# Performance work log

Measured on AMD Instinct MI355X. Metric: run time of the kernel, lower is better.

Reference implementation:

```python
import jax, jax.numpy as jnp
import numpy as np

H = 16          # num_heads
K = 15          # kernel_size (padding_l = K-1, causal)
EPS = 1e-5      # LayerNorm eps


def setup_inputs() -> dict:
    key = jax.random.key(0)
    ks = jax.random.split(key, 8)
    T, B, C, F = 1024, 8, 1024, 4096
    n = lambda k, shape, scale=1.0: jax.random.normal(k, shape, jnp.float32) * scale
    return {
        "x": n(ks[0], (T, B, C)),
        "w_lin": n(ks[1], (C, H * K), 0.02),      # dynamic-conv weight projection
        "b_lin": jnp.zeros((H * K,), jnp.float32),
        "ln_g": jnp.ones((C,), jnp.float32),
        "ln_b": jnp.zeros((C,), jnp.float32),
        "fc1_w": n(ks[2], (C, F), 0.02),
        "fc1_b": jnp.zeros((F,), jnp.float32),
        "fc2_w": n(ks[3], (F, C), 0.02),
        "fc2_b": jnp.zeros((C,), jnp.float32),
    }


def _dynamic_conv(x, w_lin, b_lin):
    # x: (T, B, C). Per-timestep weights -> softmax over kernel -> causal conv.
    T, B, C = x.shape
    R = C // H  # channels per head
    w = jnp.einsum('tbc,ck->tbk', x, w_lin) + b_lin          # (T, B, H*K)
    w = jax.nn.softmax(w.reshape(T, B, H, K), axis=-1)        # softmax over kernel taps
    # causal left-padding: tap k sees x[t + k - (K-1)]
    xp = jnp.pad(x, ((K - 1, 0), (0, 0), (0, 0))).reshape(T + K - 1, B, H, R)
    o = jnp.zeros((T, B, H, R), x.dtype)
    for k in range(K):  # fixed small kernel loop; avoids (T,B,C,K) unfold tensor
        o = o + w[:, :, :, k:k + 1] * xp[k:k + T]
    return o.reshape(T, B, C)


def _layer_norm(y, g, b):
    mu = jnp.mean(y, axis=-1, keepdims=True)
    var = jnp.var(y, axis=-1, keepdims=True)
    return (y - mu) * jax.lax.rsqrt(var + EPS) * g + b


def _forward(x, w_lin, b_lin, ln_g, ln_b, fc1_w, fc1_b, fc2_w, fc2_b):
    y = _dynamic_conv(x, w_lin, b_lin)
    y = _layer_norm(y, ln_g, ln_b)
    h = jax.nn.relu(jnp.einsum('tbc,cf->tbf', y, fc1_w) + fc1_b)
    out = jnp.einsum('tbf,fc->tbc', h, fc2_w) + fc2_b
    return out + y  # residual around FFN (residual taken post-LayerNorm)


def reference(x, w_lin, b_lin, ln_g, ln_b, fc1_w, fc1_b, fc2_w, fc2_b):
    return _forward(x, w_lin, b_lin, ln_g, ln_b, fc1_w, fc1_b, fc2_w, fc2_b)
```

## Files before the change

kernel.cpp:

```cpp
#include <hip/hip_runtime.h>


#define T_DIM 1024
#define B_DIM 8
#define C_DIM 1024
#define F_DIM 4096
#define H_DIM 16
#define K_TAP 15
#define TB (T_DIM * B_DIM)

typedef __attribute__((ext_vector_type(8))) short short8;
typedef __attribute__((ext_vector_type(4))) float f32x4;

__device__ __forceinline__ float bf2f(unsigned short u) {
    union { unsigned int i; float f; } v; v.i = ((unsigned int)u) << 16; return v.f;
}
__device__ __forceinline__ unsigned short f2bf(float f) {
    union { float f; unsigned int i; } v; v.f = f;
    unsigned int r = v.i + 0x7fffu + ((v.i >> 16) & 1u);
    return (unsigned short)(r >> 16);
}

__device__ __forceinline__ void async_copy16(const void* gptr, void* lptr) {
    __builtin_amdgcn_global_load_lds(
        (const __attribute__((address_space(1))) void*)gptr,
        (__attribute__((address_space(3))) void*)lptr, 16, 0, 0);
}

__global__ __launch_bounds__(256)
void prep(const float* __restrict__ x, unsigned short* __restrict__ xb,
          const float* __restrict__ fc1_w, unsigned short* __restrict__ fc1T,
          const float* __restrict__ fc2_w, unsigned short* __restrict__ fc2T,
          const float* __restrict__ w_lin, unsigned short* __restrict__ wlinT) {
    const int bid = blockIdx.x;
    const int tid = threadIdx.x;
    if (bid < 8192) {
        int i = (bid * 256 + tid) * 4;
        float4 v = *(const float4*)(x + i);
        uint2 o;
        o.x = (unsigned int)f2bf(v.x) | ((unsigned int)f2bf(v.y) << 16);
        o.y = (unsigned int)f2bf(v.z) | ((unsigned int)f2bf(v.w) << 16);
        *(uint2*)(xb + i) = o;
        return;
    }
    const float* in; unsigned short* out; int R, Cin, c0, r0;
    if (bid < 12288) {
        int idx = bid - 8192;
        in = fc1_w; out = fc1T; R = C_DIM; Cin = F_DIM;
        c0 = (idx & 127) * 32; r0 = (idx >> 7) * 32;
    } else if (bid < 16384) {
        int idx = bid - 12288;
        in = fc2_w; out = fc2T; R = F_DIM; Cin = C_DIM;
        c0 = (idx & 31) * 32; r0 = (idx >> 5) * 32;
    } else {
        int idx = bid - 16384;
        in = w_lin; out = wlinT; R = C_DIM; Cin = 240;
        c0 = (idx & 7) * 32; r0 = (idx >> 3) * 32;
    }
    __shared__ unsigned short tile[32][33];
    const int xx = tid & 31, yy = tid >> 5;
#pragma unroll
    for (int j = 0; j < 4; j++) {
        int r = r0 + yy + j * 8, c = c0 + xx;
        unsigned short v = 0;
        if (c < Cin) v = f2bf(in[(size_t)r * Cin + c]);
        tile[yy + j * 8][xx] = v;
    }
    __syncthreads();
#pragma unroll
    for (int j = 0; j < 4; j++) {
        out[(size_t)(c0 + yy + j * 8) * R + (r0 + xx)] = tile[xx][yy + j * 8];
    }
}

template <int MODE, int SWAP>
__global__ __launch_bounds__(256)
void gemm_bt(const unsigned short* __restrict__ A,
             const unsigned short* __restrict__ Bt,
             void* __restrict__ Cout_v,
             int M, int N, int K, int kz,
             const float* __restrict__ bias,
             const unsigned short* __restrict__ resid) {
    __shared__ __align__(16) unsigned short As[2][128 * 64];
    __shared__ __align__(16) unsigned short Bs[2][128 * 64];

    const int tid = threadIdx.x;
    const int m0 = (SWAP ? blockIdx.x : blockIdx.y) * 128;
    const int n0 = (SWAP ? blockIdx.y : blockIdx.x) * 128;
    const int kbase = blockIdx.z * kz;
    const int wave = tid >> 6, lane = tid & 63;
    const int quad = lane >> 4, l16 = lane & 15;
    const int wm = (wave >> 1) * 64;
    const int wn = (wave & 1) * 64;

    f32x4 acc[4][4];
#pragma unroll
    for (int i = 0; i < 4; i++)
#pragma unroll
        for (int j = 0; j < 4; j++) acc[i][j] = (f32x4){0.f, 0.f, 0.f, 0.f};

    const int rsub = lane >> 3;
    const int gch = (lane & 7) ^ rsub;
    const unsigned short* gA = A + (size_t)(m0 + wave * 32 + rsub) * K + kbase + gch * 8;
    const unsigned short* gB = Bt + (size_t)(n0 + wave * 32 + rsub) * K + kbase + gch * 8;
    unsigned short* lA[2] = {&As[0][wave * 32 * 64], &As[1][wave * 32 * 64]};
    unsigned short* lB[2] = {&Bs[0][wave * 32 * 64], &Bs[1][wave * 32 * 64]};

#pragma unroll
    for (int j = 0; j < 4; j++) {
        async_copy16(gA + (size_t)j * 8 * K, lA[0] + j * 8 * 64);
        async_copy16(gB + (size_t)j * 8 * K, lB[0] + j * 8 * 64);
    }

    const int swz = l16 & 7;
    int buf = 0;
    for (int k0 = 0; k0 < kz; k0 += 64) {
        __syncthreads();

        const int nk = k0 + 64;
        if (nk < kz) {
            const int nb = buf ^ 1;
#pragma unroll
            for (int j = 0; j < 4; j++) {
                async_copy16(gA + nk + (size_t)j * 8 * K, lA[nb] + j * 8 * 64);
                async_copy16(gB + nk + (size_t)j * 8 * K, lB[nb] + j * 8 * 64);
            }
        }

        short8 af[2][4], bfr[2][4];
#pragma unroll
        for (int kk = 0; kk < 2; kk++) {
            const int c = kk * 4 + quad;
#pragma unroll
            for (int i = 0; i < 4; i++) {
                af[kk][i]  = *(const short8*)(&As[buf][(wm + i * 16 + l16) * 64 + (c ^ swz) * 8]);
                bfr[kk][i] = *(const short8*)(&Bs[buf][(wn + i * 16 + l16) * 64 + (c ^ swz) * 8]);
            }
        }
#pragma unroll
        for (int kk = 0; kk < 2; kk++)
#pragma unroll
            for (int mi = 0; mi < 4; mi++)
#pragma unroll
                for (int nj = 0; nj < 4; nj++)
                    acc[mi][nj] = __builtin_amdgcn_mfma_f32_16x16x32_bf16(
                        af[kk][mi], bfr[kk][nj], acc[mi][nj], 0, 0, 0);
        buf ^= 1;
    }

    const int crow0 = m0 + wm + quad * 4;
    const int ccol0 = n0 + wn + l16;
    if (MODE == 3) {
        float* Cf = (float*)Cout_v + (size_t)blockIdx.z * M * N;
#pragma unroll
        for (int mi = 0; mi < 4; mi++)
#pragma unroll
            for (int i = 0; i < 4; i++) {
                int rr = crow0 + mi * 16 + i;
#pragma unroll
                for (int nj = 0; nj < 4; nj++)
                    Cf[(size_t)rr * N + ccol0 + nj * 16] = acc[mi][nj][i];
            }
    } else if (MODE == 1) {
        unsigned short* Cb = (unsigned short*)Cout_v;
        float bv[4];
#pragma unroll
        for (int nj = 0; nj < 4; nj++) bv[nj] = bias[ccol0 + nj * 16];
#pragma unroll
        for (int mi = 0; mi < 4; mi++)
#pragma unroll
            for (int i = 0; i < 4; i++) {
                int rr = crow0 + mi * 16 + i;
#pragma unroll
                for (int nj = 0; nj < 4; nj++) {
                    float v = fmaxf(acc[mi][nj][i] + bv[nj], 0.f);
                    Cb[(size_t)rr * N + ccol0 + nj * 16] = f2bf(v);
                }
            }
    } else {
        float* Cf = (float*)Cout_v;
        float bv[4];
#pragma unroll
        for (int nj = 0; nj < 4; nj++) bv[nj] = bias[ccol0 + nj * 16];
#pragma unroll
        for (int mi = 0; mi < 4; mi++)
#pragma unroll
            for (int i = 0; i < 4; i++) {
                int rr = crow0 + mi * 16 + i;
#pragma unroll
                for (int nj = 0; nj < 4; nj++) {
                    float v = acc[mi][nj][i] + bv[nj]
                            + bf2f(resid[(size_t)rr * N + ccol0 + nj * 16]);
                    Cf[(size_t)rr * N + ccol0 + nj * 16] = v;
                }
            }
    }
}

#define WS_STRIDE ((size_t)TB * 256)
__global__ __launch_bounds__(256)
void conv_ln8s(const unsigned short* __restrict__ x,
               const float* __restrict__ wscore,
               const float* __restrict__ b_lin,
               const float* __restrict__ ln_g,
               const float* __restrict__ ln_b,
               unsigned short* __restrict__ y) {
    __shared__ __align__(16) unsigned short xs[22][C_DIM];
    __shared__ float wls[8 * 240];
    const int blk = blockIdx.x;
    const int b = blk & 7;
    const int t0 = (blk >> 3) * 8;
    const int tid = threadIdx.x;

    if (tid < 128) {
        const int rj = tid >> 4, hh = tid & 15;
        const size_t row = (size_t)(t0 + rj) * B_DIM + b;
        const float* p = wscore + row * 256 + hh * 15;
        float v[K_TAP], mx = -1e30f;
#pragma unroll
        for (int k = 0; k < K_TAP; k++) {
            v[k] = p[k] + p[k + WS_STRIDE] + p[k + 2 * WS_STRIDE] + p[k + 3 * WS_STRIDE]
                 + b_lin[hh * K_TAP + k];
            mx = fmaxf(mx, v[k]);
        }
        float s = 0.f;
#pragma unroll
        for (int k = 0; k < K_TAP; k++) { v[k] = __expf(v[k] - mx); s += v[k]; }
        float inv = 1.0f / s;
#pragma unroll
        for (int k = 0; k < K_TAP; k++) wls[rj * 240 + hh * K_TAP + k] = v[k] * inv;
    }

#pragma unroll
    for (int k = 0; k < 22; k++) {
        int t = t0 + k - 14;
        uint2 val = make_uint2(0u, 0u);
        if (t >= 0)
            val = *(const uint2*)(x + ((size_t)t * B_DIM + b) * C_DIM + tid * 4);
        *(uint2*)(&xs[k][tid * 4]) = val;
    }
    __syncthreads();

    const int wave = tid >> 6, lane = tid & 63;
    const int ch0 = lane * 16;
    const int h = lane >> 2;

    for (int rj = wave; rj < 8; rj += 4) {
        float acc[16];
#pragma unroll
        for (int i = 0; i < 16; i++) acc[i] = 0.f;
#pragma unroll
        for (int k = 0; k < K_TAP; k++) {
            float w = wls[rj * 240 + h * 15 + k];
            const unsigned short* xr = &xs[rj + k][ch0];
            uint4 p0 = *(const uint4*)(xr);
            uint4 p1 = *(const uint4*)(xr + 8);
            unsigned int uu[8] = {p0.x, p0.y, p0.z, p0.w, p1.x, p1.y, p1.z, p1.w};
#pragma unroll
            for (int q = 0; q < 8; q++) {
                acc[2 * q]     += w * bf2f((unsigned short)(uu[q] & 0xffff));
                acc[2 * q + 1] += w * bf2f((unsigned short)(uu[q] >> 16));
            }
        }
        float s = 0.f, s2 = 0.f;
#pragma unroll
        for (int i = 0; i < 16; i++) { s += acc[i]; s2 += acc[i] * acc[i]; }
#pragma unroll
        for (int off = 32; off > 0; off >>= 1) {
            s  += __shfl_xor(s, off, 64);
            s2 += __shfl_xor(s2, off, 64);
        }
        float mu = s * (1.0f / C_DIM);
        float var = s2 * (1.0f / C_DIM) - mu * mu;
        float rs = rsqrtf(var + 1e-5f);

        unsigned short o16[16];
#pragma unroll
        for (int i = 0; i < 16; i++)
            o16[i] = f2bf((acc[i] - mu) * rs * ln_g[ch0 + i] + ln_b[ch0 + i]);
        uint4 w0, w1;
        w0.x = (unsigned int)o16[0]  | ((unsigned int)o16[1]  << 16);
        w0.y = (unsigned int)o16[2]  | ((unsigned int)o16[3]  << 16);
        w0.z = (unsigned int)o16[4]  | ((unsigned int)o16[5]  << 16);
        w0.w = (unsigned int)o16[6]  | ((unsigned int)o16[7]  << 16);
        w1.x = (unsigned int)o16[8]  | ((unsigned int)o16[9]  << 16);
        w1.y = (unsigned int)o16[10] | ((unsigned int)o16[11] << 16);
        w1.z = (unsigned int)o16[12] | ((unsigned int)o16[13] << 16);
        w1.w = (unsigned int)o16[14] | ((unsigned int)o16[15] << 16);
        unsigned short* yr = y + ((size_t)(t0 + rj) * B_DIM + b) * C_DIM + ch0;
        *(uint4*)(yr) = w0;
        *(uint4*)(yr + 8) = w1;
    }
}

extern "C" void kernel_launch(void* const* d_in, const int* in_sizes, int n_in,
                              void* d_out, int out_size, void* d_ws, size_t ws_size,
                              hipStream_t stream) {
    const float* x     = (const float*)d_in[0];
    const float* w_lin = (const float*)d_in[1];
    const float* b_lin = (const float*)d_in[2];
    const float* ln_g  = (const float*)d_in[3];
    const float* ln_b  = (const float*)d_in[4];
    const float* fc1_w = (const float*)d_in[5];
    const float* fc1_b = (const float*)d_in[6];
    const float* fc2_w = (const float*)d_in[7];
    const float* fc2_b = (const float*)d_in[8];
    float* out = (float*)d_out;

    char* ws = (char*)d_ws;
    unsigned short* xb    = (unsigned short*)(ws);
    unsigned short* fc1T  = (unsigned short*)(ws + 16777216);
    unsigned short* fc2T  = (unsigned short*)(ws + 25165824);
    unsigned short* wlinT = (unsigned short*)(ws + 33554432);
    unsigned short* y     = (unsigned short*)(ws + 34078720);
    unsigned short* h     = (unsigned short*)(ws + 50855936);
    float* wscore = (float*)(ws + 50855936);

    prep<<<16640, 256, 0, stream>>>(x, xb, fc1_w, fc1T, fc2_w, fc2T, w_lin, wlinT);

    gemm_bt<3, 0><<<dim3(256 / 128, TB / 128, 4), 256, 0, stream>>>(
        xb, wlinT, (void*)wscore, TB, 256, C_DIM, C_DIM / 4, nullptr, nullptr);

    conv_ln8s<<<TB / 8, 256, 0, stream>>>(xb, wscore, b_lin, ln_g, ln_b, y);

    gemm_bt<1, 0><<<dim3(F_DIM / 128, TB / 128, 1), 256, 0, stream>>>(
        y, fc1T, (void*)h, TB, F_DIM, C_DIM, C_DIM, fc1_b, nullptr);

    gemm_bt<2, 1><<<dim3(TB / 128, C_DIM / 128, 1), 256, 0, stream>>>(
        h, fc2T, (void*)out, TB, C_DIM, F_DIM, F_DIM, fc2_b, y);
}
```

Before: 316.0 us.

## Fuse dynamic-conv weight projection GEMM into conv+LayerNorm kernel

Removes the split-K weight-score GEMM and its fp32 partial-sum workspace. The conv kernel now computes the per-timestep tap scores itself with MFMA, using 16 timesteps per block staged in padded shared memory, then applies softmax, the causal conv and LayerNorm. This saves a kernel launch and the global round trip of the score partials. In exchange, every block reads the full w_lin weight from global/L2 without LDS staging, and shared memory use per block grows.

```diff
diff --git a/kernel.cpp b/kernel.cpp
--- a/kernel.cpp
+++ b/kernel.cpp
@@ -78,7 +78,7 @@
 void gemm_bt(const unsigned short* __restrict__ A,
              const unsigned short* __restrict__ Bt,
              void* __restrict__ Cout_v,
-             int M, int N, int K, int kz,
+             int M, int N, int K,
              const float* __restrict__ bias,
              const unsigned short* __restrict__ resid) {
     __shared__ __align__(16) unsigned short As[2][128 * 64];
@@ -87,7 +87,6 @@
     const int tid = threadIdx.x;
     const int m0 = (SWAP ? blockIdx.x : blockIdx.y) * 128;
     const int n0 = (SWAP ? blockIdx.y : blockIdx.x) * 128;
-    const int kbase = blockIdx.z * kz;
     const int wave = tid >> 6, lane = tid & 63;
     const int quad = lane >> 4, l16 = lane & 15;
     const int wm = (wave >> 1) * 64;
@@ -101,8 +100,8 @@
 
     const int rsub = lane >> 3;
     const int gch = (lane & 7) ^ rsub;
-    const unsigned short* gA = A + (size_t)(m0 + wave * 32 + rsub) * K + kbase + gch * 8;
-    const unsigned short* gB = Bt + (size_t)(n0 + wave * 32 + rsub) * K + kbase + gch * 8;
+    const unsigned short* gA = A + (size_t)(m0 + wave * 32 + rsub) * K + gch * 8;
+    const unsigned short* gB = Bt + (size_t)(n0 + wave * 32 + rsub) * K + gch * 8;
     unsigned short* lA[2] = {&As[0][wave * 32 * 64], &As[1][wave * 32 * 64]};
     unsigned short* lB[2] = {&Bs[0][wave * 32 * 64], &Bs[1][wave * 32 * 64]};
 
@@ -114,11 +113,11 @@
 
     const int swz = l16 & 7;
     int buf = 0;
-    for (int k0 = 0; k0 < kz; k0 += 64) {
+    for (int k0 = 0; k0 < K; k0 += 64) {
         __syncthreads();
 
         const int nk = k0 + 64;
-        if (nk < kz) {
+        if (nk < K) {
             const int nb = buf ^ 1;
 #pragma unroll
             for (int j = 0; j < 4; j++) {
@@ -150,18 +149,7 @@
 
     const int crow0 = m0 + wm + quad * 4;
     const int ccol0 = n0 + wn + l16;
-    if (MODE == 3) {
-        float* Cf = (float*)Cout_v + (size_t)blockIdx.z * M * N;
-#pragma unroll
-        for (int mi = 0; mi < 4; mi++)
-#pragma unroll
-            for (int i = 0; i < 4; i++) {
-                int rr = crow0 + mi * 16 + i;
-#pragma unroll
-                for (int nj = 0; nj < 4; nj++)
-                    Cf[(size_t)rr * N + ccol0 + nj * 16] = acc[mi][nj][i];
-            }
-    } else if (MODE == 1) {
+    if (MODE == 1) {
         unsigned short* Cb = (unsigned short*)Cout_v;
         float bv[4];
 #pragma unroll
@@ -197,30 +185,60 @@
     }
 }
 
-#define WS_STRIDE ((size_t)TB * 256)
+#define XSP 1032
 __global__ __launch_bounds__(256)
-void conv_ln8s(const unsigned short* __restrict__ x,
-               const float* __restrict__ wscore,
-               const float* __restrict__ b_lin,
-               const float* __restrict__ ln_g,
-               const float* __restrict__ ln_b,
-               unsigned short* __restrict__ y) {
-    __shared__ __align__(16) unsigned short xs[22][C_DIM];
-    __shared__ float wls[8 * 240];
+void conv_fused(const unsigned short* __restrict__ xb,
+                const unsigned short* __restrict__ wlinT,
+                const float* __restrict__ b_lin,
+                const float* __restrict__ ln_g,
+                const float* __restrict__ ln_b,
+                unsigned short* __restrict__ y) {
+    __shared__ __align__(16) unsigned short xs[30 * XSP];
+    __shared__ float sc[16 * 256];
     const int blk = blockIdx.x;
     const int b = blk & 7;
-    const int t0 = (blk >> 3) * 8;
+    const int t0 = (blk >> 3) * 16;
     const int tid = threadIdx.x;
 
-    if (tid < 128) {
-        const int rj = tid >> 4, hh = tid & 15;
-        const size_t row = (size_t)(t0 + rj) * B_DIM + b;
-        const float* p = wscore + row * 256 + hh * 15;
+#pragma unroll
+    for (int j = 0; j < 30; j++) {
+        int t = t0 + j - 14;
+        uint2 val = make_uint2(0u, 0u);
+        if (t >= 0)
+            val = *(const uint2*)(xb + ((size_t)t * B_DIM + b) * C_DIM + tid * 4);
+        *(uint2*)(&xs[j * XSP + tid * 4]) = val;
+    }
+    __syncthreads();
+
+    const int wave = tid >> 6, lane = tid & 63;
+    const int quad = lane >> 4, l16 = lane & 15;
+
+    f32x4 acc[4];
+#pragma unroll
+    for (int nt = 0; nt < 4; nt++) acc[nt] = (f32x4){0.f, 0.f, 0.f, 0.f};
+    for (int ki = 0; ki < 32; ki++) {
+        short8 a = *(const short8*)(&xs[(14 + l16) * XSP + ki * 32 + quad * 8]);
+#pragma unroll
+        for (int nt = 0; nt < 4; nt++) {
+            int n = (wave * 4 + nt) * 16 + l16;
+            short8 bf = *(const short8*)(wlinT + (size_t)n * C_DIM + ki * 32 + quad * 8);
+            acc[nt] = __builtin_amdgcn_mfma_f32_16x16x32_bf16(a, bf, acc[nt], 0, 0, 0);
+        }
+    }
+#pragma unroll
+    for (int nt = 0; nt < 4; nt++)
+#pragma unroll
+        for (int i = 0; i < 4; i++)
+            sc[(quad * 4 + i) * 256 + (wave * 4 + nt) * 16 + l16] = acc[nt][i];
+    __syncthreads();
+
+    {
+        const int row = tid >> 4, hh = tid & 15;
+        float* p = &sc[row * 256 + hh * K_TAP];
         float v[K_TAP], mx = -1e30f;
 #pragma unroll
         for (int k = 0; k < K_TAP; k++) {
-            v[k] = p[k] + p[k + WS_STRIDE] + p[k + 2 * WS_STRIDE] + p[k + 3 * WS_STRIDE]
-                 + b_lin[hh * K_TAP + k];
+            v[k] = p[k] + b_lin[hh * K_TAP + k];
             mx = fmaxf(mx, v[k]);
         }
         float s = 0.f;
@@ -228,43 +246,32 @@
         for (int k = 0; k < K_TAP; k++) { v[k] = __expf(v[k] - mx); s += v[k]; }
         float inv = 1.0f / s;
 #pragma unroll
-        for (int k = 0; k < K_TAP; k++) wls[rj * 240 + hh * K_TAP + k] = v[k] * inv;
-    }
-
-#pragma unroll
-    for (int k = 0; k < 22; k++) {
-        int t = t0 + k - 14;
-        uint2 val = make_uint2(0u, 0u);
-        if (t >= 0)
-            val = *(const uint2*)(x + ((size_t)t * B_DIM + b) * C_DIM + tid * 4);
-        *(uint2*)(&xs[k][tid * 4]) = val;
+        for (int k = 0; k < K_TAP; k++) p[k] = v[k] * inv;
     }
     __syncthreads();
 
-    const int wave = tid >> 6, lane = tid & 63;
     const int ch0 = lane * 16;
     const int h = lane >> 2;
-
-    for (int rj = wave; rj < 8; rj += 4) {
-        float acc[16];
-#pragma unroll
-        for (int i = 0; i < 16; i++) acc[i] = 0.f;
+    for (int rj = wave; rj < 16; rj += 4) {
+        float o[16];
+#pragma unroll
+        for (int i = 0; i < 16; i++) o[i] = 0.f;
 #pragma unroll
         for (int k = 0; k < K_TAP; k++) {
-            float w = wls[rj * 240 + h * 15 + k];
-            const unsigned short* xr = &xs[rj + k][ch0];
+            float w = sc[rj * 256 + h * K_TAP + k];
+            const unsigned short* xr = &xs[(rj + k) * XSP + ch0];
             uint4 p0 = *(const uint4*)(xr);
             uint4 p1 = *(const uint4*)(xr + 8);
             unsigned int uu[8] = {p0.x, p0.y, p0.z, p0.w, p1.x, p1.y, p1.z, p1.w};
 #pragma unroll
             for (int q = 0; q < 8; q++) {
-                acc[2 * q]     += w * bf2f((unsigned short)(uu[q] & 0xffff));
-                acc[2 * q + 1] += w * bf2f((unsigned short)(uu[q] >> 16));
+                o[2 * q]     += w * bf2f((unsigned short)(uu[q] & 0xffff));
+                o[2 * q + 1] += w * bf2f((unsigned short)(uu[q] >> 16));
             }
         }
         float s = 0.f, s2 = 0.f;
 #pragma unroll
-        for (int i = 0; i < 16; i++) { s += acc[i]; s2 += acc[i] * acc[i]; }
+        for (int i = 0; i < 16; i++) { s += o[i]; s2 += o[i] * o[i]; }
 #pragma unroll
         for (int off = 32; off > 0; off >>= 1) {
             s  += __shfl_xor(s, off, 64);
@@ -277,7 +284,7 @@
         unsigned short o16[16];
 #pragma unroll
         for (int i = 0; i < 16; i++)
-            o16[i] = f2bf((acc[i] - mu) * rs * ln_g[ch0 + i] + ln_b[ch0 + i]);
+            o16[i] = f2bf((o[i] - mu) * rs * ln_g[ch0 + i] + ln_b[ch0 + i]);
         uint4 w0, w1;
         w0.x = (unsigned int)o16[0]  | ((unsigned int)o16[1]  << 16);
         w0.y = (unsigned int)o16[2]  | ((unsigned int)o16[3]  << 16);
@@ -314,18 +321,14 @@
     unsigned short* wlinT = (unsigned short*)(ws + 33554432);
     unsigned short* y     = (unsigned short*)(ws + 34078720);
     unsigned short* h     = (unsigned short*)(ws + 50855936);
-    float* wscore = (float*)(ws + 50855936);
 
     prep<<<16640, 256, 0, stream>>>(x, xb, fc1_w, fc1T, fc2_w, fc2T, w_lin, wlinT);
 
-    gemm_bt<3, 0><<<dim3(256 / 128, TB / 128, 4), 256, 0, stream>>>(
-        xb, wlinT, (void*)wscore, TB, 256, C_DIM, C_DIM / 4, nullptr, nullptr);
-
-    conv_ln8s<<<TB / 8, 256, 0, stream>>>(xb, wscore, b_lin, ln_g, ln_b, y);
-
-    gemm_bt<1, 0><<<dim3(F_DIM / 128, TB / 128, 1), 256, 0, stream>>>(
-        y, fc1T, (void*)h, TB, F_DIM, C_DIM, C_DIM, fc1_b, nullptr);
-
-    gemm_bt<2, 1><<<dim3(TB / 128, C_DIM / 128, 1), 256, 0, stream>>>(
-        h, fc2T, (void*)out, TB, C_DIM, F_DIM, F_DIM, fc2_b, y);
-}
+    conv_fused<<<TB / 16, 256, 0, stream>>>(xb, wlinT, b_lin, ln_g, ln_b, y);
+
+    gemm_bt<1, 0><<<dim3(F_DIM / 128, TB / 128), 256, 0, stream>>>(
+        y, fc1T, (void*)h, TB, F_DIM, C_DIM, fc1_b, nullptr);
+
+    gemm_bt<2, 1><<<dim3(TB / 128, C_DIM / 128), 256, 0, stream>>>(
+        h, fc2T, (void*)out, TB, C_DIM, F_DIM, fc2_b, y);
+}
```

New measurement: 328.6 us. +4.0%, slower.
